# Kernel optimization log

Measured on AMD Instinct MI355X. Metric: run time of the kernel, lower is better.

## Reference

```python
import jax, jax.numpy as jnp
import numpy as np

N_NODES = 100000
N_EDGES = 3200000
IN_CH = 64
HID = [64, 32, 16]


def setup_inputs() -> dict:
    key = jax.random.key(0)
    ks = jax.random.split(key, 12)
    x = jax.random.normal(ks[0], (N_NODES, IN_CH), dtype=jnp.float32)
    edge_index = jax.random.randint(ks[1], (2, N_EDGES), 0, N_NODES, dtype=jnp.int32)
    dims = [IN_CH] + HID
    params = {}
    i = 2
    for l in range(3):
        din, dout = dims[l], dims[l + 1]
        sc = 1.0 / np.sqrt(din)
        params[f"Wl{l}"] = jax.random.uniform(ks[i], (din, dout), jnp.float32, -sc, sc); i += 1
        params[f"Wr{l}"] = jax.random.uniform(ks[i], (din, dout), jnp.float32, -sc, sc); i += 1
        params[f"b{l}"] = jnp.zeros((dout,), jnp.float32)
    sc = 1.0 / np.sqrt(HID[-1])
    params["Wc"] = jax.random.uniform(ks[i], (HID[-1], 1), jnp.float32, -sc, sc)
    params["bc"] = jnp.zeros((1,), jnp.float32)
    return dict(x=x, edge_index=edge_index, **params)


def _sage_conv(x, src, dst, Wl, Wr, b):
    # message = x[src]; mean-aggregate at dst; out = agg @ Wl + x @ Wr + b
    msg = x[src]  # [E, din]
    s = jax.ops.segment_sum(msg, dst, num_segments=N_NODES)
    cnt = jax.ops.segment_sum(jnp.ones((dst.shape[0],), x.dtype), dst, num_segments=N_NODES)
    agg = s / jnp.maximum(cnt, 1.0)[:, None]
    return agg @ Wl + x @ Wr + b


def reference(x, edge_index, Wl0, Wr0, b0, Wl1, Wr1, b1, Wl2, Wr2, b2, Wc, bc):
    src, dst = edge_index[0], edge_index[1]
    h = jax.nn.relu(_sage_conv(x, src, dst, Wl0, Wr0, b0))
    h = jax.nn.relu(_sage_conv(h, src, dst, Wl1, Wr1, b1))
    h = jax.nn.relu(_sage_conv(h, src, dst, Wl2, Wr2, b2))
    return h @ Wc + bc  # [N_NODES, 1]
```

## Files before the change

### kernel.cpp

```cpp
#include <hip/hip_runtime.h>


#define NN 100000
#define BSH 9
#define NBK ((NN + 511) >> 9)
#define HB 256
#define SRCMASK 0x1FFFF
#define DLSH 17

__device__ __forceinline__ unsigned f2bf(float f) {
    unsigned u = __float_as_uint(f);
    u += 0x7fffu + ((u >> 16) & 1u);
    return u >> 16;
}
__device__ __forceinline__ float bflo(unsigned u) { return __uint_as_float(u << 16); }
__device__ __forceinline__ float bfhi(unsigned u) { return __uint_as_float(u & 0xffff0000u); }

__global__ void part1_k(const int* __restrict__ src, const int* __restrict__ dst,
                        int E, int* __restrict__ gcnt, int* __restrict__ goff,
                        unsigned* __restrict__ pair) {
    __shared__ int lh[NBK];
    __shared__ int part[512];
    int c = blockIdx.x, tid = threadIdx.x;
    int chunk = (E + HB - 1) / HB;
    int b0 = c * chunk, e0 = min(b0 + chunk, E);
    if (tid < NBK) lh[tid] = 0;
    __syncthreads();
    for (int e = b0 + tid; e < e0; e += 512) atomicAdd(&lh[dst[e] >> BSH], 1);
    __syncthreads();
    int cnt = (tid < NBK) ? lh[tid] : 0;
    part[tid] = cnt;
    __syncthreads();
    for (int d = 1; d < 512; d <<= 1) {
        int t = (tid >= d) ? part[tid - d] : 0;
        __syncthreads();
        part[tid] += t;
        __syncthreads();
    }
    int run = (tid == 0) ? 0 : part[tid - 1];
    if (tid < NBK) {
        gcnt[(size_t)c * NBK + tid] = cnt;
        goff[(size_t)c * NBK + tid] = run;
        lh[tid] = run;
    }
    __syncthreads();
    for (int e = b0 + tid; e < e0; e += 512) {
        int dv = dst[e], sv = src[e];
        int p = b0 + atomicAdd(&lh[dv >> BSH], 1);
        pair[p] = (unsigned)sv | ((unsigned)(dv & 511) << DLSH);
    }
}

__global__ void bsum_k(const int* __restrict__ gcnt, int* __restrict__ bb, int E) {
    __shared__ int part[256];
    int tid = threadIdx.x;
    int s = 0;
    if (tid < NBK)
        for (int c = 0; c < HB; ++c) s += gcnt[(size_t)c * NBK + tid];
    part[tid] = s;
    __syncthreads();
    for (int d = 1; d < 256; d <<= 1) {
        int t = (tid >= d) ? part[tid - d] : 0;
        __syncthreads();
        part[tid] += t;
        __syncthreads();
    }
    if (tid < NBK) bb[tid] = part[tid] - s;
    if (tid == 0) bb[NBK] = E;
}

__global__ void sort2_k(const unsigned* __restrict__ pair, const int* __restrict__ goff,
                        const int* __restrict__ bb, int* __restrict__ adj,
                        int* __restrict__ off, float* __restrict__ inv, int N, int E) {
    __shared__ int sls[HB], sle[HB];
    __shared__ int lcnt[512], lcur[512];
    __shared__ int part[256];
    int b = blockIdx.x, tid = threadIdx.x;
    int chunk = (E + HB - 1) / HB;
    int b0c = tid * chunk, e0c = min(b0c + chunk, E);
    sls[tid] = b0c + goff[(size_t)tid * NBK + b];
    sle[tid] = (b + 1 < NBK) ? (b0c + goff[(size_t)tid * NBK + b + 1]) : e0c;
    lcnt[tid] = 0; lcnt[tid + 256] = 0;
    __syncthreads();
    for (int i = sls[tid]; i < sle[tid]; ++i)
        atomicAdd(&lcnt[pair[i] >> DLSH], 1);
    __syncthreads();
    int c0 = lcnt[2 * tid], c1 = lcnt[2 * tid + 1];
    part[tid] = c0 + c1;
    __syncthreads();
    for (int d = 1; d < 256; d <<= 1) {
        int t = (tid >= d) ? part[tid - d] : 0;
        __syncthreads();
        part[tid] += t;
        __syncthreads();
    }
    int run = (tid == 0) ? 0 : part[tid - 1];
    int base = bb[b];
    int v0 = b << BSH;
    int vg0 = v0 + 2 * tid, vg1 = v0 + 2 * tid + 1;
    if (vg0 < N) { off[vg0] = base + run;      inv[vg0] = 1.f / (float)max(c0, 1); }
    if (vg1 < N) { off[vg1] = base + run + c0; inv[vg1] = 1.f / (float)max(c1, 1); }
    lcur[2 * tid] = base + run;
    lcur[2 * tid + 1] = base + run + c0;
    if (b == NBK - 1 && tid == 0) off[N] = E;
    __syncthreads();
    for (int i = sls[tid]; i < sle[tid]; ++i) {
        unsigned u = pair[i];
        int p = atomicAdd(&lcur[u >> DLSH], 1);
        adj[p] = u & SRCMASK;
    }
}

template <int DIN, int DOUT>
__global__ void transform2_k(const float* __restrict__ h,
                             const float* __restrict__ Wl, const float* __restrict__ Wr,
                             const float* __restrict__ bias,
                             unsigned* __restrict__ g, float2* __restrict__ r, int N) {
    constexpr int JP = DOUT / 2;
    __shared__ float2 sWl[DIN * JP];
    __shared__ float2 sWr[DIN * JP];
    __shared__ float2 sb[JP];
    const float2* Wl2 = (const float2*)Wl;
    const float2* Wr2 = (const float2*)Wr;
    for (int i = threadIdx.x; i < DIN * JP; i += blockDim.x) { sWl[i] = Wl2[i]; sWr[i] = Wr2[i]; }
    if (threadIdx.x < JP) sb[threadIdx.x] = ((const float2*)bias)[threadIdx.x];
    __syncthreads();
    int idx = blockIdx.x * blockDim.x + threadIdx.x;
    int NP = N / 2;
    if (idx >= NP * JP) return;
    int p = idx / JP, jp = idx % JP;
    int v0 = 2 * p, v1 = v0 + 1;
    const float* h0 = h + (size_t)v0 * DIN;
    const float* h1 = h + (size_t)v1 * DIN;
    float gl0x = 0, gl0y = 0, gl1x = 0, gl1y = 0;
    float gr0x = 0, gr0y = 0, gr1x = 0, gr1y = 0;
#pragma unroll
    for (int k = 0; k < DIN; ++k) {
        float2 wl = sWl[k * JP + jp];
        float2 wr = sWr[k * JP + jp];
        float a0 = h0[k], a1 = h1[k];
        gl0x = fmaf(a0, wl.x, gl0x); gl0y = fmaf(a0, wl.y, gl0y);
        gl1x = fmaf(a1, wl.x, gl1x); gl1y = fmaf(a1, wl.y, gl1y);
        gr0x = fmaf(a0, wr.x, gr0x); gr0y = fmaf(a0, wr.y, gr0y);
        gr1x = fmaf(a1, wr.x, gr1x); gr1y = fmaf(a1, wr.y, gr1y);
    }
    float2 bb = sb[jp];
    g[(size_t)v0 * JP + jp] = f2bf(gl0x) | (f2bf(gl0y) << 16);
    g[(size_t)v1 * JP + jp] = f2bf(gl1x) | (f2bf(gl1y) << 16);
    r[(size_t)v0 * JP + jp] = make_float2(gr0x + bb.x, gr0y + bb.y);
    r[(size_t)v1 * JP + jp] = make_float2(gr1x + bb.x, gr1y + bb.y);
}

template <int DOUT, int WAVES, int HEAD>
__global__ void agg_k(const unsigned* __restrict__ g, const int* __restrict__ off,
                      const int* __restrict__ adj, const float* __restrict__ invc,
                      const float* r, const float* __restrict__ Wc,
                      const float* __restrict__ bc, float* out, int N) {
    constexpr int Q8 = DOUT / 8;
    constexpr int EPT = 64 / Q8;
    __shared__ float sagg[WAVES][DOUT];
    int wid = threadIdx.x >> 6, lane = threadIdx.x & 63;
    int v = blockIdx.x * WAVES + wid;
    bool active = v < N;
    int q = lane & (Q8 - 1);
    int eg = lane / Q8;
    float acc[8] = {0, 0, 0, 0, 0, 0, 0, 0};
#define ACCU(U) do { \
        acc[0] += bflo(U.x); acc[1] += bfhi(U.x); \
        acc[2] += bflo(U.y); acc[3] += bfhi(U.y); \
        acc[4] += bflo(U.z); acc[5] += bfhi(U.z); \
        acc[6] += bflo(U.w); acc[7] += bfhi(U.w); } while (0)
    if (active) {
        int beg = off[v], end = off[v + 1];
        const uint4* g4 = (const uint4*)g;
        int i = beg + eg;
        for (; i + 3 * EPT < end; i += 4 * EPT) {
            int s0 = adj[i], s1 = adj[i + EPT], s2 = adj[i + 2 * EPT], s3 = adj[i + 3 * EPT];
            uint4 u0 = g4[(size_t)s0 * Q8 + q];
            uint4 u1 = g4[(size_t)s1 * Q8 + q];
            uint4 u2 = g4[(size_t)s2 * Q8 + q];
            uint4 u3 = g4[(size_t)s3 * Q8 + q];
            ACCU(u0); ACCU(u1); ACCU(u2); ACCU(u3);
        }
        for (; i < end; i += EPT) {
            int sv = adj[i];
            uint4 u = g4[(size_t)sv * Q8 + q];
            ACCU(u);
        }
#pragma unroll
        for (int d = Q8; d < 64; d <<= 1)
#pragma unroll
            for (int c = 0; c < 8; ++c) acc[c] += __shfl_xor(acc[c], d, 64);
        if (eg == 0) {
            float4* sp = (float4*)&sagg[wid][q * 8];
            sp[0] = make_float4(acc[0], acc[1], acc[2], acc[3]);
            sp[1] = make_float4(acc[4], acc[5], acc[6], acc[7]);
        }
    }
#undef ACCU
    __syncthreads();
    if (active && lane < DOUT) {
        float iv = invc[v];
        float val = fmaxf(fmaf(sagg[wid][lane], iv, r[(size_t)v * DOUT + lane]), 0.f);
        if (!HEAD) {
            out[(size_t)v * DOUT + lane] = val;
        } else {
            float pp = val * Wc[lane];
#pragma unroll
            for (int d = 1; d < 16; d <<= 1) pp += __shfl_xor(pp, d, 64);
            if (lane == 0) out[v] = pp + bc[0];
        }
    }
}

extern "C" void kernel_launch(void* const* d_in, const int* in_sizes, int n_in,
                              void* d_out, int out_size, void* d_ws, size_t ws_size,
                              hipStream_t stream) {
    const float* x   = (const float*)d_in[0];
    const int*   ei  = (const int*)d_in[1];
    const float* Wl0 = (const float*)d_in[2];
    const float* Wr0 = (const float*)d_in[3];
    const float* b0  = (const float*)d_in[4];
    const float* Wl1 = (const float*)d_in[5];
    const float* Wr1 = (const float*)d_in[6];
    const float* b1  = (const float*)d_in[7];
    const float* Wl2 = (const float*)d_in[8];
    const float* Wr2 = (const float*)d_in[9];
    const float* b2  = (const float*)d_in[10];
    const float* Wc  = (const float*)d_in[11];
    const float* bc  = (const float*)d_in[12];
    float* out = (float*)d_out;

    const int N = NN;
    const int E = in_sizes[1] / 2;
    const int* src = ei;
    const int* dst = ei + E;

    char* ws = (char*)d_ws;
    const size_t MB = 1 << 20;
    int*      gcnt = (int*)(ws + 0);
    int*      goff = (int*)(ws + 1 * MB);
    int*      bb   = (int*)(ws + 2 * MB);
    int*      off  = (int*)(ws + 3 * MB);
    float*    inv  = (float*)(ws + 3 * MB + 512 * 1024);
    unsigned* pair = (unsigned*)(ws + 4 * MB);
    int*      adj  = (int*)(ws + 17 * MB);
    unsigned* g0 = (unsigned*)(ws + 30 * MB);
    float*    r0 = (float*)(ws + 43 * MB);
    float*    h1 = r0;
    unsigned* g1 = (unsigned*)(ws + 4 * MB);
    float*    r1 = (float*)(ws + 30 * MB);
    float*    h2 = r1;
    unsigned* g2 = (unsigned*)(ws + 11 * MB);
    float*    r2 = (float*)(ws + 43 * MB);

    part1_k<<<HB, 512, 0, stream>>>(src, dst, E, gcnt, goff, pair);
    bsum_k<<<1, 256, 0, stream>>>(gcnt, bb, E);
    sort2_k<<<NBK, HB, 0, stream>>>(pair, goff, bb, adj, off, inv, N, E);

    transform2_k<64, 64><<<(N / 2 * 32 + 255) / 256, 256, 0, stream>>>(x, Wl0, Wr0, b0, g0, (float2*)r0, N);
    agg_k<64, 4, 0><<<(N + 3) / 4, 256, 0, stream>>>(g0, off, adj, inv, r0, nullptr, nullptr, h1, N);

    transform2_k<64, 32><<<(N / 2 * 16 + 255) / 256, 256, 0, stream>>>(h1, Wl1, Wr1, b1, g1, (float2*)r1, N);
    agg_k<32, 4, 0><<<(N + 3) / 4, 256, 0, stream>>>(g1, off, adj, inv, r1, nullptr, nullptr, h2, N);

    transform2_k<32, 16><<<(N / 2 * 8 + 255) / 256, 256, 0, stream>>>(h2, Wl2, Wr2, b2, g2, (float2*)r2, N);
    agg_k<16, 4, 1><<<(N + 3) / 4, 256, 0, stream>>>(g2, off, adj, inv, r2, Wc, bc, out, N);
}
```

Baseline: 434.3 us.

## Stage bucket scatter in shared memory and shrink bucket size to 256 nodes

The partition kernel now scatters (src,dst) pairs into a shared-memory buffer and then writes them to global memory contiguously. The sort kernel builds each bucket's adjacency in shared memory, with a global fallback past capacity, and writes it out coalesced. Buckets are halved to 256 nodes, so there are more sort blocks and the bucket-sum scan runs 512 wide. This removes scattered global writes, at the cost of more shared memory per block (about 50KB in part1) and lower occupancy.

Result: faster. 405.4 us (-6.7%).

```diff
diff --git a/kernel.cpp b/kernel.cpp
--- a/kernel.cpp
+++ b/kernel.cpp
@@ -2,11 +2,13 @@
 
 
 #define NN 100000
-#define BSH 9
-#define NBK ((NN + 511) >> 9)
+#define BSH 8
+#define NBK ((NN + 255) >> 8)
 #define HB 256
 #define SRCMASK 0x1FFFF
 #define DLSH 17
+#define SPCAP 12500
+#define LADJ_CAP 10240
 
 __device__ __forceinline__ unsigned f2bf(float f) {
     unsigned u = __float_as_uint(f);
@@ -19,11 +21,13 @@
 __global__ void part1_k(const int* __restrict__ src, const int* __restrict__ dst,
                         int E, int* __restrict__ gcnt, int* __restrict__ goff,
                         unsigned* __restrict__ pair) {
+    __shared__ unsigned spair[SPCAP];
     __shared__ int lh[NBK];
     __shared__ int part[512];
     int c = blockIdx.x, tid = threadIdx.x;
     int chunk = (E + HB - 1) / HB;
     int b0 = c * chunk, e0 = min(b0 + chunk, E);
+    int n = e0 - b0;
     if (tid < NBK) lh[tid] = 0;
     __syncthreads();
     for (int e = b0 + tid; e < e0; e += 512) atomicAdd(&lh[dst[e] >> BSH], 1);
@@ -46,20 +50,22 @@
     __syncthreads();
     for (int e = b0 + tid; e < e0; e += 512) {
         int dv = dst[e], sv = src[e];
-        int p = b0 + atomicAdd(&lh[dv >> BSH], 1);
-        pair[p] = (unsigned)sv | ((unsigned)(dv & 511) << DLSH);
-    }
+        int p = atomicAdd(&lh[dv >> BSH], 1);
+        spair[p] = (unsigned)sv | ((unsigned)(dv & 255) << DLSH);
+    }
+    __syncthreads();
+    for (int i = tid; i < n; i += 512) pair[b0 + i] = spair[i];
 }
 
 __global__ void bsum_k(const int* __restrict__ gcnt, int* __restrict__ bb, int E) {
-    __shared__ int part[256];
+    __shared__ int part[512];
     int tid = threadIdx.x;
     int s = 0;
     if (tid < NBK)
         for (int c = 0; c < HB; ++c) s += gcnt[(size_t)c * NBK + tid];
     part[tid] = s;
     __syncthreads();
-    for (int d = 1; d < 256; d <<= 1) {
+    for (int d = 1; d < 512; d <<= 1) {
         int t = (tid >= d) ? part[tid - d] : 0;
         __syncthreads();
         part[tid] += t;
@@ -72,21 +78,23 @@
 __global__ void sort2_k(const unsigned* __restrict__ pair, const int* __restrict__ goff,
                         const int* __restrict__ bb, int* __restrict__ adj,
                         int* __restrict__ off, float* __restrict__ inv, int N, int E) {
+    __shared__ int ladj[LADJ_CAP];
     __shared__ int sls[HB], sle[HB];
-    __shared__ int lcnt[512], lcur[512];
+    __shared__ int lcur[256];
     __shared__ int part[256];
     int b = blockIdx.x, tid = threadIdx.x;
     int chunk = (E + HB - 1) / HB;
     int b0c = tid * chunk, e0c = min(b0c + chunk, E);
-    sls[tid] = b0c + goff[(size_t)tid * NBK + b];
-    sle[tid] = (b + 1 < NBK) ? (b0c + goff[(size_t)tid * NBK + b + 1]) : e0c;
-    lcnt[tid] = 0; lcnt[tid + 256] = 0;
-    __syncthreads();
-    for (int i = sls[tid]; i < sle[tid]; ++i)
-        atomicAdd(&lcnt[pair[i] >> DLSH], 1);
-    __syncthreads();
-    int c0 = lcnt[2 * tid], c1 = lcnt[2 * tid + 1];
-    part[tid] = c0 + c1;
+    int ls = b0c + goff[(size_t)tid * NBK + b];
+    int le = (b + 1 < NBK) ? (b0c + goff[(size_t)tid * NBK + b + 1]) : e0c;
+    sls[tid] = ls; sle[tid] = le;
+    lcur[tid] = 0;
+    __syncthreads();
+    for (int i = ls; i < le; ++i)
+        atomicAdd(&lcur[pair[i] >> DLSH], 1);
+    __syncthreads();
+    int cn = lcur[tid];
+    part[tid] = cn;
     __syncthreads();
     for (int d = 1; d < 256; d <<= 1) {
         int t = (tid >= d) ? part[tid - d] : 0;
@@ -94,21 +102,24 @@
         part[tid] += t;
         __syncthreads();
     }
-    int run = (tid == 0) ? 0 : part[tid - 1];
+    int run = part[tid] - cn;
     int base = bb[b];
-    int v0 = b << BSH;
-    int vg0 = v0 + 2 * tid, vg1 = v0 + 2 * tid + 1;
-    if (vg0 < N) { off[vg0] = base + run;      inv[vg0] = 1.f / (float)max(c0, 1); }
-    if (vg1 < N) { off[vg1] = base + run + c0; inv[vg1] = 1.f / (float)max(c1, 1); }
-    lcur[2 * tid] = base + run;
-    lcur[2 * tid + 1] = base + run + c0;
+    int total = bb[b + 1] - base;
+    int v = (b << BSH) + tid;
+    if (v < N) { off[v] = base + run; inv[v] = 1.f / (float)max(cn, 1); }
     if (b == NBK - 1 && tid == 0) off[N] = E;
+    lcur[tid] = run;
     __syncthreads();
     for (int i = sls[tid]; i < sle[tid]; ++i) {
         unsigned u = pair[i];
         int p = atomicAdd(&lcur[u >> DLSH], 1);
-        adj[p] = u & SRCMASK;
-    }
+        int val = u & SRCMASK;
+        if (p < LADJ_CAP) ladj[p] = val;
+        else adj[base + p] = val;
+    }
+    __syncthreads();
+    int lim = min(total, LADJ_CAP);
+    for (int i = tid; i < lim; i += 256) adj[base + i] = ladj[i];
 }
 
 template <int DIN, int DOUT>
@@ -255,7 +266,7 @@
     float*    r2 = (float*)(ws + 43 * MB);
 
     part1_k<<<HB, 512, 0, stream>>>(src, dst, E, gcnt, goff, pair);
-    bsum_k<<<1, 256, 0, stream>>>(gcnt, bb, E);
+    bsum_k<<<1, 512, 0, stream>>>(gcnt, bb, E);
     sort2_k<<<NBK, HB, 0, stream>>>(pair, goff, bb, adj, off, inv, N, E);
 
     transform2_k<64, 64><<<(N / 2 * 32 + 255) / 256, 256, 0, stream>>>(x, Wl0, Wr0, b0, g0, (float2*)r0, N);
```
